# Optimization experiments

Hardware: AMD Instinct MI355X
Metric: run time of the kernel (lower is better)

Reference implementation:

```python
import jax, jax.numpy as jnp
import numpy as np

B, T, D, H, NB = 4, 2048, 128, 4, 2
DK = D // H
LN_EPS = 1e-3  # keras LayerNormalization default epsilon


def _pos_encoding(maxlen, d):
    # faithful to TransformerNet.get_position_encoding (flat pos-major layout)
    pe = np.array([pos / np.power(10000, 2 * i / d) for pos in range(maxlen) for i in range(d)])
    pe[::2] = np.sin(pe[::2])
    pe[1::2] = np.cos(pe[1::2])
    return jnp.asarray(pe.reshape(maxlen, d), dtype=jnp.float32)


def _ln(x, g, b):
    mu = jnp.mean(x, axis=-1, keepdims=True)
    var = jnp.mean(jnp.square(x - mu), axis=-1, keepdims=True)
    return g * (x - mu) / jnp.sqrt(var + LN_EPS) + b


def setup_inputs() -> dict:
    key = jax.random.key(0)
    ks = jax.random.split(key, 14)
    s = 1.0 / np.sqrt(D)
    w = lambda k, shape: (jax.random.normal(k, shape, jnp.float32) * s)
    return {
        'inputs': jax.random.normal(ks[0], (B, T, D), jnp.float32),
        'Wq': w(ks[1], (NB, D, D)), 'bq': jnp.zeros((NB, D), jnp.float32),
        'Wk': w(ks[2], (NB, D, D)), 'bk': jnp.zeros((NB, D), jnp.float32),
        'Wv': w(ks[3], (NB, D, D)), 'bv': jnp.zeros((NB, D), jnp.float32),
        'Wo': w(ks[4], (NB, D, D)), 'bo': jnp.zeros((NB, D), jnp.float32),
        'W1': w(ks[5], (NB, D, D)), 'b1': jnp.zeros((NB, D), jnp.float32),
        'W2': w(ks[6], (NB, D, D)), 'b2': jnp.zeros((NB, D), jnp.float32),
        'ln_g': jnp.ones((2 * NB, D), jnp.float32),
        'ln_b': jnp.zeros((2 * NB, D), jnp.float32),
    }


def reference(inputs, Wq, bq, Wk, bk, Wv, bv, Wo, bo, W1, b1, W2, b2, ln_g, ln_b):
    h = inputs + _pos_encoding(T, D)[None]  # [B,T,D]
    scale = 1.0 / jnp.sqrt(jnp.float32(DK))
    for i in range(NB):
        # pre-attention LayerNorm
        h = _ln(h, ln_g[2 * i], ln_b[2 * i])
        q = (h @ Wq[i] + bq[i]).reshape(B, T, H, DK)
        k = (h @ Wk[i] + bk[i]).reshape(B, T, H, DK)
        v = (h @ Wv[i] + bv[i]).reshape(B, T, H, DK)
        scores = jnp.einsum('bqhd,bkhd->bhqk', q, k) * scale
        p = jax.nn.softmax(scores, axis=-1)
        # mask is None in TransformerNet.call, but the renormalize step remains
        attn = p / (jnp.sum(p, axis=-1, keepdims=True) + 1e-8)
        ctx = jnp.einsum('bhqk,bkhd->bqhd', attn, v).reshape(B, T, D)
        h = ctx @ Wo[i] + bo[i]  # no residual around attention (as in source)
        # pre-FFN LayerNorm
        h = _ln(h, ln_g[2 * i + 1], ln_b[2 * i + 1])
        # FeedForward with internal residual
        h = h + (jnp.maximum(h @ W1[i] + b1[i], 0.0) @ W2[i] + b2[i])
    # final norm reuses norm_layers[-1] == norm_layers[2*NB-1] (source quirk)
    return _ln(h, ln_g[-1], ln_b[-1])
```

## Files before the change

kernel.cpp:

```cpp
#include <hip/hip_runtime.h>
#include <hip/hip_bf16.h>

typedef __bf16 bf16x8 __attribute__((ext_vector_type(8)));
typedef __bf16 bf16x4 __attribute__((ext_vector_type(4)));
typedef float f32x4 __attribute__((ext_vector_type(4)));
typedef float f32x16 __attribute__((ext_vector_type(16)));
typedef unsigned int u32x4v __attribute__((ext_vector_type(4)));

#define D_ 128
#define T_ 2048
#define B_ 4
#define H_ 4
#define NB_ 2


__global__ __launch_bounds__(256) void prep_weights(
    const float* __restrict__ Wq, const float* __restrict__ Wk,
    const float* __restrict__ Wv, const float* __restrict__ Wo,
    const float* __restrict__ W1, const float* __restrict__ W2,
    __bf16* __restrict__ wp)
{
  int tid = blockIdx.x * 256 + threadIdx.x;
  int e    = tid & 7;
  int lane = (tid >> 3) & 63;
  int ks   = (tid >> 9) & 3;
  int nt   = (tid >> 11) & 7;
  int i    = (tid >> 14) & (NB_ - 1);
  int j    = tid >> 15;
  int k = ks * 32 + (lane >> 4) * 8 + e;
  int n = nt * 16 + (lane & 15);
  const float* srcs[6] = {Wq, Wk, Wv, Wo, W1, W2};
  wp[tid] = (__bf16)srcs[j][i * 16384 + k * 128 + n];
}

__global__ __launch_bounds__(256) void posadd(
    const float* __restrict__ x, __bf16* __restrict__ hp)
{
  int w = threadIdx.x >> 6, lane = threadIdx.x & 63;
  int row = blockIdx.x * 4 + w;
  int t = row & (T_ - 1);
  #pragma unroll
  for (int e = 0; e < 2; e++) {
    int c = lane * 2 + e;
    float arg = (float)t * exp2f(-0.20762050593045952f * (float)c);
    float pe = (c & 1) ? cosf(arg) : sinf(arg);
    float v = x[row * D_ + c] + pe;
    size_t idx = ((size_t)(row >> 4) * 4 + (c >> 5)) * 512 +
                 ((row & 15) + 16 * ((c >> 3) & 3)) * 8 + (c & 7);
    hp[idx] = (__bf16)v;
  }
}

__global__ __launch_bounds__(256) void lnqkv(
    const __bf16* __restrict__ hp, const __bf16* __restrict__ wpq,
    const __bf16* __restrict__ wpk, const __bf16* __restrict__ wpv,
    const float* __restrict__ bq, const float* __restrict__ bk,
    const float* __restrict__ bv, const float* __restrict__ g,
    const float* __restrict__ beta,
    __bf16* __restrict__ qp, __bf16* __restrict__ kp, __bf16* __restrict__ vp)
{
  int w = threadIdx.x >> 6, lane = threadIdx.x & 63;
  int m0 = blockIdx.x * 16;
  int lr = lane & 15, kg = lane >> 4;

  bf16x8 araw[4];
  #pragma unroll
  for (int ks = 0; ks < 4; ks++)
    araw[ks] = *(const bf16x8*)(hp + ((size_t)blockIdx.x * 4 + ks) * 512 + lane * 8);

  float s = 0.f, s2 = 0.f;
  #pragma unroll
  for (int ks = 0; ks < 4; ks++)
    #pragma unroll
    for (int e = 0; e < 8; e++) {
      float x = (float)araw[ks][e];
      s += x; s2 += x * x;
    }
  s += __shfl_xor(s, 16, 64);  s2 += __shfl_xor(s2, 16, 64);
  s += __shfl_xor(s, 32, 64);  s2 += __shfl_xor(s2, 32, 64);
  float mu = s * (1.f / D_);
  float var = s2 * (1.f / D_) - mu * mu;
  float rstd = rsqrtf(var + 1e-3f);

  bf16x8 af[4];
  #pragma unroll
  for (int ks = 0; ks < 4; ks++) {
    int c0 = ks * 32 + kg * 8;
    float4 g0 = *(const float4*)(g + c0), g1 = *(const float4*)(g + c0 + 4);
    float4 q0 = *(const float4*)(beta + c0), q1 = *(const float4*)(beta + c0 + 4);
    const float* gp[2] = {&g0.x, &g1.x};
    const float* bp[2] = {&q0.x, &q1.x};
    #pragma unroll
    for (int e = 0; e < 8; e++)
      af[ks][e] = (__bf16)(((float)araw[ks][e] - mu) * rstd * gp[e >> 2][e & 3] + bp[e >> 2][e & 3]);
  }

  #pragma unroll
  for (int i = 0; i < 2; i++) {
    int nt = w * 2 + i;
    const __bf16* wq = wpq + (size_t)(nt * 4) * 512 + lane * 8;
    const __bf16* wk = wpk + (size_t)(nt * 4) * 512 + lane * 8;
    const __bf16* wv = wpv + (size_t)(nt * 4) * 512 + lane * 8;
    f32x4 aq = {0, 0, 0, 0}, ak = {0, 0, 0, 0}, av = {0, 0, 0, 0};
    #pragma unroll
    for (int ks = 0; ks < 4; ks++) {
      aq = __builtin_amdgcn_mfma_f32_16x16x32_bf16(af[ks], *(const bf16x8*)(wq + ks * 512), aq, 0, 0, 0);
      ak = __builtin_amdgcn_mfma_f32_16x16x32_bf16(af[ks], *(const bf16x8*)(wk + ks * 512), ak, 0, 0, 0);
      av = __builtin_amdgcn_mfma_f32_16x16x32_bf16(af[ks], *(const bf16x8*)(wv + ks * 512), av, 0, 0, 0);
    }
    int col = nt * 16 + lr;
    float bqc = bq[col], bkc = bk[col], bvc = bv[col];
    int dk = i * 16 + lr;
    int hi8 = (lr >> 3) & 1;
    #pragma unroll
    for (int r = 0; r < 4; r++) {
      int row = m0 + kg * 4 + r;
      int bb = row >> 11, tt = row & (T_ - 1);
      size_t qidx = ((((size_t)(bb * 64 + (tt >> 5)) * 4 + w) * 2 + i) * 512) +
                    ((tt & 31) + 32 * hi8) * 8 + (lr & 7);
      qp[qidx] = (__bf16)(aq[r] + bqc);
      size_t kidx = ((((size_t)(bb * 4 + w) * 64 + (tt >> 5)) * 2 + i) * 512) +
                    ((tt & 31) + 32 * hi8) * 8 + (lr & 7);
      kp[kidx] = (__bf16)(ak[r] + bkc);
      size_t vidx = ((((size_t)(bb * 4 + w) * 64 + (tt >> 5)) * 2 + ((tt >> 4) & 1)) * 512) +
                    (dk + 32 * ((tt >> 3) & 1)) * 8 + (tt & 7);
      vp[vidx] = (__bf16)(av[r] + bvc);
    }
  }
}

__global__ __launch_bounds__(256) void attn7(
    const __bf16* __restrict__ qp, const __bf16* __restrict__ kp,
    const __bf16* __restrict__ vp, __bf16* __restrict__ cp)
{
  __shared__ float mbuf[3][64][17];

  int w = threadIdx.x >> 6, lane = threadIdx.x & 63;
  int bh = blockIdx.x & 15, qt = blockIdx.x >> 4;
  int b = bh >> 2, h = bh & 3;
  int lq = lane & 31, hi = lane >> 5;

  const float qscale = 0.17677669529663687f * 1.4426950408889634f;
  const __bf16* qbase = qp + (((size_t)(b * 64 + qt) * 4 + h) * 2) * 512 + lane * 8;
  bf16x8 qraw0 = *(const bf16x8*)(qbase);
  bf16x8 qraw1 = *(const bf16x8*)(qbase + 512);
  bf16x8 qf0, qf1;
  #pragma unroll
  for (int e = 0; e < 8; e++) {
    qf0[e] = (__bf16)((float)qraw0[e] * qscale);
    qf1[e] = (__bf16)((float)qraw1[e] * qscale);
  }

  const __bf16* kbase = kp + ((size_t)(b * 4 + h) * 64) * 1024 + lane * 8;
  const __bf16* vbase = vp + ((size_t)(b * 4 + h) * 64) * 1024 + lane * 8;

  f32x16 acc;
  #pragma unroll
  for (int r = 0; r < 16; r++) acc[r] = 0.f;
  float l = 0.f;

  int kt = w * 16;
  bf16x8 kf0 = *(const bf16x8*)(kbase + (size_t)kt * 1024);
  bf16x8 kf1 = *(const bf16x8*)(kbase + (size_t)kt * 1024 + 512);
  bf16x8 vf0 = *(const bf16x8*)(vbase + (size_t)kt * 1024);
  bf16x8 vf1 = *(const bf16x8*)(vbase + (size_t)kt * 1024 + 512);

  for (int it = 0; it < 16; it++) {
    __builtin_amdgcn_s_setprio(1);
    f32x16 s;
    #pragma unroll
    for (int r = 0; r < 16; r++) s[r] = -24.f;
    s = __builtin_amdgcn_mfma_f32_32x32x16_bf16(kf0, qf0, s, 0, 0, 0);
    s = __builtin_amdgcn_mfma_f32_32x32x16_bf16(kf1, qf1, s, 0, 0, 0);
    __builtin_amdgcn_s_setprio(0);

    bf16x8 kn0, kn1, vn0, vn1;
    if (it < 15) {
      size_t nb = (size_t)(kt + 1) * 1024;
      kn0 = *(const bf16x8*)(kbase + nb);
      kn1 = *(const bf16x8*)(kbase + nb + 512);
      vn0 = *(const bf16x8*)(vbase + nb);
      vn1 = *(const bf16x8*)(vbase + nb + 512);
    }

    unsigned int aw[8];
    #pragma unroll
    for (int g = 0; g < 4; g++) {
      float p0 = __builtin_amdgcn_exp2f(s[g * 4 + 0]);
      float p1 = __builtin_amdgcn_exp2f(s[g * 4 + 1]);
      float p2 = __builtin_amdgcn_exp2f(s[g * 4 + 2]);
      float p3 = __builtin_amdgcn_exp2f(s[g * 4 + 3]);
      l += (p0 + p1) + (p2 + p3);
      unsigned int u01, u23;
      asm("v_cvt_pk_bf16_f32 %0, %1, %2" : "=v"(u01) : "v"(p0), "v"(p1));
      asm("v_cvt_pk_bf16_f32 %0, %1, %2" : "=v"(u23) : "v"(p2), "v"(p3));
      aw[g * 2] = u01; aw[g * 2 + 1] = u23;
    }
    unsigned int a0 = aw[0], a2 = aw[2];
    asm volatile("v_permlane32_swap_b32 %0, %1" : "+v"(a0), "+v"(a2));
    unsigned int a1 = aw[1], a3 = aw[3];
    asm volatile("v_permlane32_swap_b32 %0, %1" : "+v"(a1), "+v"(a3));
    bf16x8 pw0 = __builtin_bit_cast(bf16x8, (u32x4v){a0, a1, a2, a3});
    unsigned int a4 = aw[4], a6 = aw[6];
    asm volatile("v_permlane32_swap_b32 %0, %1" : "+v"(a4), "+v"(a6));
    unsigned int a5 = aw[5], a7 = aw[7];
    asm volatile("v_permlane32_swap_b32 %0, %1" : "+v"(a5), "+v"(a7));
    bf16x8 pw1 = __builtin_bit_cast(bf16x8, (u32x4v){a4, a5, a6, a7});

    __builtin_amdgcn_s_setprio(1);
    acc = __builtin_amdgcn_mfma_f32_32x32x16_bf16(vf0, pw0, acc, 0, 0, 0);
    acc = __builtin_amdgcn_mfma_f32_32x32x16_bf16(vf1, pw1, acc, 0, 0, 0);
    __builtin_amdgcn_s_setprio(0);

    kf0 = kn0; kf1 = kn1; vf0 = vn0; vf1 = vn1;
    kt += 1;
  }

  l += __shfl_xor(l, 32, 64);

  if (w > 0) {
    float* mb = &mbuf[w - 1][lane][0];
    #pragma unroll
    for (int r = 0; r < 16; r++) mb[r] = acc[r];
    mb[16] = l;
  }
  __syncthreads();
  if (w == 0) {
    #pragma unroll
    for (int w2_ = 0; w2_ < 3; w2_++) {
      const float* mb = &mbuf[w2_][lane][0];
      #pragma unroll
      for (int r = 0; r < 16; r++) acc[r] += mb[r];
      l += mb[16];
    }
    float inv = 1.f / l;
    __bf16* cbase = cp + ((size_t)(b * 128 + qt * 2 + (lq >> 4)) * 4 + h) * 512 + 4 * hi;
    #pragma unroll
    for (int g = 0; g < 4; g++) {
      bf16x4 o;
      #pragma unroll
      for (int j = 0; j < 4; j++) o[j] = (__bf16)(acc[g * 4 + j] * inv);
      *(bf16x4*)(cbase + ((lq & 15) + 16 * g) * 8) = o;
    }
  }
}

template <int LAST>
__global__ __launch_bounds__(256) void wo_ffn(
    const __bf16* __restrict__ cp, const __bf16* __restrict__ wpo,
    const float* __restrict__ bo, const float* __restrict__ g1,
    const float* __restrict__ bt1, const __bf16* __restrict__ wp1,
    const float* __restrict__ b1, const __bf16* __restrict__ wp2,
    const float* __restrict__ b2, const float* __restrict__ g2,
    const float* __restrict__ bt2, __bf16* __restrict__ hp,
    float* __restrict__ outf)
{
  __shared__ __attribute__((aligned(16))) __bf16 tb0[16][128];
  __shared__ __attribute__((aligned(16))) __bf16 tb1[16][128];
  __shared__ float2 statb[16][4];

  int w = threadIdx.x >> 6, lane = threadIdx.x & 63;
  int m0 = blockIdx.x * 16;
  int lr = lane & 15, kg = lane >> 4;
  int swz = (lr & 7) << 3;

  bf16x8 af[4];
  #pragma unroll
  for (int ks = 0; ks < 4; ks++)
    af[ks] = *(const bf16x8*)(cp + ((size_t)blockIdx.x * 4 + ks) * 512 + lane * 8);

  f32x4 acc[2] = {{0, 0, 0, 0}, {0, 0, 0, 0}};
  #pragma unroll
  for (int i = 0; i < 2; i++) {
    const __bf16* wrow = wpo + (size_t)((w * 2 + i) * 4) * 512 + lane * 8;
    #pragma unroll
    for (int ks = 0; ks < 4; ks++)
      acc[i] = __builtin_amdgcn_mfma_f32_16x16x32_bf16(af[ks], *(const bf16x8*)(wrow + ks * 512), acc[i], 0, 0, 0);
  }

  float xv[2][4];
  float s[4] = {0, 0, 0, 0}, s2[4] = {0, 0, 0, 0};
  #pragma unroll
  for (int i = 0; i < 2; i++) {
    float bcol = bo[(w * 2 + i) * 16 + lr];
    #pragma unroll
    for (int r = 0; r < 4; r++) {
      float y = acc[i][r] + bcol;
      xv[i][r] = y; s[r] += y; s2[r] += y * y;
    }
  }
  #pragma unroll
  for (int r = 0; r < 4; r++)
    for (int mk = 1; mk < 16; mk <<= 1) {
      s[r] += __shfl_xor(s[r], mk, 64);
      s2[r] += __shfl_xor(s2[r], mk, 64);
    }
  if (lr == 0) {
    #pragma unroll
    for (int r = 0; r < 4; r++) statb[kg * 4 + r][w] = make_float2(s[r], s2[r]);
  }
  __syncthreads();
  float mu_[4], rstd_[4];
  #pragma unroll
  for (int r = 0; r < 4; r++) {
    int row = kg * 4 + r;
    float ss = 0.f, ss2 = 0.f;
    #pragma unroll
    for (int w2 = 0; w2 < 4; w2++) {
      float2 t = statb[row][w2];
      ss += t.x; ss2 += t.y;
    }
    mu_[r] = ss * (1.f / D_);
    float var = ss2 * (1.f / D_) - mu_[r] * mu_[r];
    rstd_[r] = rsqrtf(var + 1e-3f);
  }
  float hres[2][4];
  #pragma unroll
  for (int i = 0; i < 2; i++) {
    int col = (w * 2 + i) * 16 + lr;
    float gc = g1[col], bc = bt1[col];
    #pragma unroll
    for (int r = 0; r < 4; r++) {
      float y = (xv[i][r] - mu_[r]) * rstd_[r] * gc + bc;
      hres[i][r] = y;
      int row = kg * 4 + r;
      tb0[row][col ^ ((row & 7) << 3)] = (__bf16)y;
    }
  }
  __syncthreads();

  bf16x8 a2[4];
  #pragma unroll
  for (int ks = 0; ks < 4; ks++)
    a2[ks] = *(const bf16x8*)(&tb0[lr][(ks * 32 + kg * 8) ^ swz]);
  f32x4 acc2[2] = {{0, 0, 0, 0}, {0, 0, 0, 0}};
  #pragma unroll
  for (int i = 0; i < 2; i++) {
    const __bf16* wrow = wp1 + (size_t)((w * 2 + i) * 4) * 512 + lane * 8;
    #pragma unroll
    for (int ks = 0; ks < 4; ks++)
      acc2[i] = __builtin_amdgcn_mfma_f32_16x16x32_bf16(a2[ks], *(const bf16x8*)(wrow + ks * 512), acc2[i], 0, 0, 0);
  }
  #pragma unroll
  for (int i = 0; i < 2; i++) {
    float bcol = b1[(w * 2 + i) * 16 + lr];
    int col = (w * 2 + i) * 16 + lr;
    #pragma unroll
    for (int r = 0; r < 4; r++) {
      int row = kg * 4 + r;
      tb1[row][col ^ ((row & 7) << 3)] = (__bf16)fmaxf(acc2[i][r] + bcol, 0.f);
    }
  }
  __syncthreads();

  bf16x8 a3[4];
  #pragma unroll
  for (int ks = 0; ks < 4; ks++)
    a3[ks] = *(const bf16x8*)(&tb1[lr][(ks * 32 + kg * 8) ^ swz]);
  f32x4 acc3[2] = {{0, 0, 0, 0}, {0, 0, 0, 0}};
  #pragma unroll
  for (int i = 0; i < 2; i++) {
    const __bf16* wrow = wp2 + (size_t)((w * 2 + i) * 4) * 512 + lane * 8;
    #pragma unroll
    for (int ks = 0; ks < 4; ks++)
      acc3[i] = __builtin_amdgcn_mfma_f32_16x16x32_bf16(a3[ks], *(const bf16x8*)(wrow + ks * 512), acc3[i], 0, 0, 0);
  }

  if constexpr (LAST) {
    float yv[2][4];
    float t[4] = {0, 0, 0, 0}, t2[4] = {0, 0, 0, 0};
    #pragma unroll
    for (int i = 0; i < 2; i++) {
      float bcol = b2[(w * 2 + i) * 16 + lr];
      #pragma unroll
      for (int r = 0; r < 4; r++) {
        float y = acc3[i][r] + bcol + hres[i][r];
        yv[i][r] = y; t[r] += y; t2[r] += y * y;
      }
    }
    #pragma unroll
    for (int r = 0; r < 4; r++)
      for (int mk = 1; mk < 16; mk <<= 1) {
        t[r] += __shfl_xor(t[r], mk, 64);
        t2[r] += __shfl_xor(t2[r], mk, 64);
      }
    __syncthreads();
    if (lr == 0) {
      #pragma unroll
      for (int r = 0; r < 4; r++) statb[kg * 4 + r][w] = make_float2(t[r], t2[r]);
    }
    __syncthreads();
    #pragma unroll
    for (int r = 0; r < 4; r++) {
      int row = kg * 4 + r;
      float ss = 0.f, ss2 = 0.f;
      #pragma unroll
      for (int w2 = 0; w2 < 4; w2++) {
        float2 tt = statb[row][w2];
        ss += tt.x; ss2 += tt.y;
      }
      float mu = ss * (1.f / D_);
      float var = ss2 * (1.f / D_) - mu * mu;
      float rstd = rsqrtf(var + 1e-3f);
      #pragma unroll
      for (int i = 0; i < 2; i++) {
        int col = (w * 2 + i) * 16 + lr;
        outf[(size_t)(m0 + row) * D_ + col] =
            (yv[i][r] - mu) * rstd * g2[col] + bt2[col];
      }
    }
  } else {
    #pragma unroll
    for (int i = 0; i < 2; i++) {
      int col = (w * 2 + i) * 16 + lr;
      float bcol = b2[col];
      size_t base = ((size_t)blockIdx.x * 4 + w) * 512 +
                    (size_t)16 * ((2 * i + (lr >> 3)) & 3) * 8 + (lr & 7);
      #pragma unroll
      for (int r = 0; r < 4; r++)
        hp[base + (kg * 4 + r) * 8] = (__bf16)(acc3[i][r] + bcol + hres[i][r]);
    }
  }
}

extern "C" void kernel_launch(void* const* d_in, const int* in_sizes, int n_in,
                              void* d_out, int out_size, void* d_ws, size_t ws_size,
                              hipStream_t stream)
{
  const float* inputs = (const float*)d_in[0];
  const float* Wq = (const float*)d_in[1];
  const float* bq = (const float*)d_in[2];
  const float* Wk = (const float*)d_in[3];
  const float* bk = (const float*)d_in[4];
  const float* Wv = (const float*)d_in[5];
  const float* bv = (const float*)d_in[6];
  const float* Wo = (const float*)d_in[7];
  const float* bo = (const float*)d_in[8];
  const float* W1 = (const float*)d_in[9];
  const float* b1 = (const float*)d_in[10];
  const float* W2 = (const float*)d_in[11];
  const float* b2 = (const float*)d_in[12];
  const float* ln_g = (const float*)d_in[13];
  const float* ln_b = (const float*)d_in[14];
  float* out = (float*)d_out;

  char* ws = (char*)d_ws;
  size_t off = 0;
  auto alloc = [&](size_t bytes) {
    void* p = ws + off;
    off = (off + bytes + 255) & ~(size_t)255;
    return p;
  };
  const size_t ACT = (size_t)8192 * 128 * sizeof(__bf16);
  __bf16* wp = (__bf16*)alloc((size_t)6 * NB_ * 16384 * sizeof(__bf16));
  __bf16* hp = (__bf16*)alloc(ACT);
  __bf16* qp = (__bf16*)alloc(ACT);
  __bf16* kp = (__bf16*)alloc(ACT);
  __bf16* vp = (__bf16*)alloc(ACT);
  __bf16* cb = (__bf16*)alloc(ACT);

  prep_weights<<<768, 256, 0, stream>>>(Wq, Wk, Wv, Wo, W1, W2, wp);
  posadd<<<2048, 256, 0, stream>>>(inputs, hp);

  for (int i = 0; i < NB_; i++) {
    const __bf16* wpq = wp + (size_t)(0 * NB_ + i) * 16384;
    const __bf16* wpk = wp + (size_t)(1 * NB_ + i) * 16384;
    const __bf16* wpv = wp + (size_t)(2 * NB_ + i) * 16384;
    const __bf16* wpo = wp + (size_t)(3 * NB_ + i) * 16384;
    const __bf16* wp1 = wp + (size_t)(4 * NB_ + i) * 16384;
    const __bf16* wp2 = wp + (size_t)(5 * NB_ + i) * 16384;

    lnqkv<<<512, 256, 0, stream>>>(hp, wpq, wpk, wpv,
                                   bq + i * 128, bk + i * 128, bv + i * 128,
                                   ln_g + (size_t)(2 * i) * 128, ln_b + (size_t)(2 * i) * 128,
                                   qp, kp, vp);
    attn7<<<1024, 256, 0, stream>>>(qp, kp, vp, cb);
    if (i == 0) {
      wo_ffn<0><<<512, 256, 0, stream>>>(cb, wpo, bo + i * 128,
                                         ln_g + 1 * 128, ln_b + 1 * 128,
                                         wp1, b1 + i * 128, wp2, b2 + i * 128,
                                         nullptr, nullptr, hp, nullptr);
    } else {
      wo_ffn<1><<<512, 256, 0, stream>>>(cb, wpo, bo + i * 128,
                                         ln_g + 3 * 128, ln_b + 3 * 128,
                                         wp1, b1 + i * 128, wp2, b2 + i * 128,
                                         ln_g + 3 * 128, ln_b + 3 * 128,
                                         nullptr, out);
    }
  }
}
```

Measured before the change: 157.1 us.

## Fuse block-0 FFN with block-1 LN+QKV and split attention keys over eight waves

The first block's Wo/FFN kernel now also runs the second block's pre-attention LayerNorm and Q/K/V projections. This drops one launch and the bf16 round trip of the hidden state through global memory. The attention kernel moves to 512 threads, splitting the key range over 8 waves of 8 tiles each instead of 4 waves of 16, to raise parallelism and shorten per-wave latency. The cost is a larger shared-memory reduction of eight partial accumulators, and a longer fused kernel that needs more registers.

```diff
diff --git a/kernel.cpp b/kernel.cpp
--- a/kernel.cpp
+++ b/kernel.cpp
@@ -129,11 +129,11 @@
   }
 }
 
-__global__ __launch_bounds__(256) void attn7(
+__global__ __launch_bounds__(512) void attn8(
     const __bf16* __restrict__ qp, const __bf16* __restrict__ kp,
     const __bf16* __restrict__ vp, __bf16* __restrict__ cp)
 {
-  __shared__ float mbuf[3][64][17];
+  __shared__ float mbuf[7][64][17];
 
   int w = threadIdx.x >> 6, lane = threadIdx.x & 63;
   int bh = blockIdx.x & 15, qt = blockIdx.x >> 4;
@@ -159,13 +159,13 @@
   for (int r = 0; r < 16; r++) acc[r] = 0.f;
   float l = 0.f;
 
-  int kt = w * 16;
+  int kt = w * 8;
   bf16x8 kf0 = *(const bf16x8*)(kbase + (size_t)kt * 1024);
   bf16x8 kf1 = *(const bf16x8*)(kbase + (size_t)kt * 1024 + 512);
   bf16x8 vf0 = *(const bf16x8*)(vbase + (size_t)kt * 1024);
   bf16x8 vf1 = *(const bf16x8*)(vbase + (size_t)kt * 1024 + 512);
 
-  for (int it = 0; it < 16; it++) {
+  for (int it = 0; it < 8; it++) {
     __builtin_amdgcn_s_setprio(1);
     f32x16 s;
     #pragma unroll
@@ -175,7 +175,7 @@
     __builtin_amdgcn_s_setprio(0);
 
     bf16x8 kn0, kn1, vn0, vn1;
-    if (it < 15) {
+    if (it < 7) {
       size_t nb = (size_t)(kt + 1) * 1024;
       kn0 = *(const bf16x8*)(kbase + nb);
       kn1 = *(const bf16x8*)(kbase + nb + 512);
@@ -227,7 +227,7 @@
   __syncthreads();
   if (w == 0) {
     #pragma unroll
-    for (int w2_ = 0; w2_ < 3; w2_++) {
+    for (int w2_ = 0; w2_ < 7; w2_++) {
       const float* mb = &mbuf[w2_][lane][0];
       #pragma unroll
       for (int r = 0; r < 16; r++) acc[r] += mb[r];
@@ -245,15 +245,214 @@
   }
 }
 
-template <int LAST>
-__global__ __launch_bounds__(256) void wo_ffn(
+__global__ __launch_bounds__(256) void wo_ffn_qkv(
+    const __bf16* __restrict__ cp, const __bf16* __restrict__ wpo,
+    const float* __restrict__ bo, const float* __restrict__ g1,
+    const float* __restrict__ bt1, const __bf16* __restrict__ wp1,
+    const float* __restrict__ b1, const __bf16* __restrict__ wp2,
+    const float* __restrict__ b2,
+    const float* __restrict__ gq, const float* __restrict__ btq,
+    const __bf16* __restrict__ wpq, const __bf16* __restrict__ wpk,
+    const __bf16* __restrict__ wpv,
+    const float* __restrict__ bq, const float* __restrict__ bk,
+    const float* __restrict__ bv,
+    __bf16* __restrict__ qp, __bf16* __restrict__ kp, __bf16* __restrict__ vp)
+{
+  __shared__ __attribute__((aligned(16))) __bf16 tb0[16][128];
+  __shared__ __attribute__((aligned(16))) __bf16 tb1[16][128];
+  __shared__ float2 statb[16][4];
+
+  int w = threadIdx.x >> 6, lane = threadIdx.x & 63;
+  int m0 = blockIdx.x * 16;
+  int lr = lane & 15, kg = lane >> 4;
+  int swz = (lr & 7) << 3;
+
+  bf16x8 af[4];
+  #pragma unroll
+  for (int ks = 0; ks < 4; ks++)
+    af[ks] = *(const bf16x8*)(cp + ((size_t)blockIdx.x * 4 + ks) * 512 + lane * 8);
+
+  f32x4 acc[2] = {{0, 0, 0, 0}, {0, 0, 0, 0}};
+  #pragma unroll
+  for (int i = 0; i < 2; i++) {
+    const __bf16* wrow = wpo + (size_t)((w * 2 + i) * 4) * 512 + lane * 8;
+    #pragma unroll
+    for (int ks = 0; ks < 4; ks++)
+      acc[i] = __builtin_amdgcn_mfma_f32_16x16x32_bf16(af[ks], *(const bf16x8*)(wrow + ks * 512), acc[i], 0, 0, 0);
+  }
+
+  float xv[2][4];
+  float s[4] = {0, 0, 0, 0}, s2[4] = {0, 0, 0, 0};
+  #pragma unroll
+  for (int i = 0; i < 2; i++) {
+    float bcol = bo[(w * 2 + i) * 16 + lr];
+    #pragma unroll
+    for (int r = 0; r < 4; r++) {
+      float y = acc[i][r] + bcol;
+      xv[i][r] = y; s[r] += y; s2[r] += y * y;
+    }
+  }
+  #pragma unroll
+  for (int r = 0; r < 4; r++)
+    for (int mk = 1; mk < 16; mk <<= 1) {
+      s[r] += __shfl_xor(s[r], mk, 64);
+      s2[r] += __shfl_xor(s2[r], mk, 64);
+    }
+  if (lr == 0) {
+    #pragma unroll
+    for (int r = 0; r < 4; r++) statb[kg * 4 + r][w] = make_float2(s[r], s2[r]);
+  }
+  __syncthreads();
+  float mu_[4], rstd_[4];
+  #pragma unroll
+  for (int r = 0; r < 4; r++) {
+    int row = kg * 4 + r;
+    float ss = 0.f, ss2 = 0.f;
+    #pragma unroll
+    for (int w2 = 0; w2 < 4; w2++) {
+      float2 t = statb[row][w2];
+      ss += t.x; ss2 += t.y;
+    }
+    mu_[r] = ss * (1.f / D_);
+    float var = ss2 * (1.f / D_) - mu_[r] * mu_[r];
+    rstd_[r] = rsqrtf(var + 1e-3f);
+  }
+  float hres[2][4];
+  #pragma unroll
+  for (int i = 0; i < 2; i++) {
+    int col = (w * 2 + i) * 16 + lr;
+    float gc = g1[col], bc = bt1[col];
+    #pragma unroll
+    for (int r = 0; r < 4; r++) {
+      float y = (xv[i][r] - mu_[r]) * rstd_[r] * gc + bc;
+      hres[i][r] = y;
+      int row = kg * 4 + r;
+      tb0[row][col ^ ((row & 7) << 3)] = (__bf16)y;
+    }
+  }
+  __syncthreads();
+
+  bf16x8 a2[4];
+  #pragma unroll
+  for (int ks = 0; ks < 4; ks++)
+    a2[ks] = *(const bf16x8*)(&tb0[lr][(ks * 32 + kg * 8) ^ swz]);
+  f32x4 acc2[2] = {{0, 0, 0, 0}, {0, 0, 0, 0}};
+  #pragma unroll
+  for (int i = 0; i < 2; i++) {
+    const __bf16* wrow = wp1 + (size_t)((w * 2 + i) * 4) * 512 + lane * 8;
+    #pragma unroll
+    for (int ks = 0; ks < 4; ks++)
+      acc2[i] = __builtin_amdgcn_mfma_f32_16x16x32_bf16(a2[ks], *(const bf16x8*)(wrow + ks * 512), acc2[i], 0, 0, 0);
+  }
+  #pragma unroll
+  for (int i = 0; i < 2; i++) {
+    float bcol = b1[(w * 2 + i) * 16 + lr];
+    int col = (w * 2 + i) * 16 + lr;
+    #pragma unroll
+    for (int r = 0; r < 4; r++) {
+      int row = kg * 4 + r;
+      tb1[row][col ^ ((row & 7) << 3)] = (__bf16)fmaxf(acc2[i][r] + bcol, 0.f);
+    }
+  }
+  __syncthreads();
+
+  bf16x8 a3[4];
+  #pragma unroll
+  for (int ks = 0; ks < 4; ks++)
+    a3[ks] = *(const bf16x8*)(&tb1[lr][(ks * 32 + kg * 8) ^ swz]);
+  f32x4 acc3[2] = {{0, 0, 0, 0}, {0, 0, 0, 0}};
+  #pragma unroll
+  for (int i = 0; i < 2; i++) {
+    const __bf16* wrow = wp2 + (size_t)((w * 2 + i) * 4) * 512 + lane * 8;
+    #pragma unroll
+    for (int ks = 0; ks < 4; ks++)
+      acc3[i] = __builtin_amdgcn_mfma_f32_16x16x32_bf16(a3[ks], *(const bf16x8*)(wrow + ks * 512), acc3[i], 0, 0, 0);
+  }
+
+  #pragma unroll
+  for (int i = 0; i < 2; i++) {
+    int col = (w * 2 + i) * 16 + lr;
+    float bcol = b2[col];
+    #pragma unroll
+    for (int r = 0; r < 4; r++) {
+      int row = kg * 4 + r;
+      tb0[row][col ^ ((row & 7) << 3)] = (__bf16)(acc3[i][r] + bcol + hres[i][r]);
+    }
+  }
+  __syncthreads();
+
+  bf16x8 araw[4];
+  #pragma unroll
+  for (int ks = 0; ks < 4; ks++)
+    araw[ks] = *(const bf16x8*)(&tb0[lr][(ks * 32 + kg * 8) ^ swz]);
+  float t = 0.f, t2 = 0.f;
+  #pragma unroll
+  for (int ks = 0; ks < 4; ks++)
+    #pragma unroll
+    for (int e = 0; e < 8; e++) {
+      float x = (float)araw[ks][e];
+      t += x; t2 += x * x;
+    }
+  t += __shfl_xor(t, 16, 64);  t2 += __shfl_xor(t2, 16, 64);
+  t += __shfl_xor(t, 32, 64);  t2 += __shfl_xor(t2, 32, 64);
+  float mu = t * (1.f / D_);
+  float var = t2 * (1.f / D_) - mu * mu;
+  float rstd = rsqrtf(var + 1e-3f);
+
+  bf16x8 af2[4];
+  #pragma unroll
+  for (int ks = 0; ks < 4; ks++) {
+    int c0 = ks * 32 + kg * 8;
+    float4 g0 = *(const float4*)(gq + c0), g1v = *(const float4*)(gq + c0 + 4);
+    float4 q0 = *(const float4*)(btq + c0), q1 = *(const float4*)(btq + c0 + 4);
+    const float* gp[2] = {&g0.x, &g1v.x};
+    const float* bp[2] = {&q0.x, &q1.x};
+    #pragma unroll
+    for (int e = 0; e < 8; e++)
+      af2[ks][e] = (__bf16)(((float)araw[ks][e] - mu) * rstd * gp[e >> 2][e & 3] + bp[e >> 2][e & 3]);
+  }
+
+  #pragma unroll
+  for (int i = 0; i < 2; i++) {
+    int nt = w * 2 + i;
+    const __bf16* wq = wpq + (size_t)(nt * 4) * 512 + lane * 8;
+    const __bf16* wk = wpk + (size_t)(nt * 4) * 512 + lane * 8;
+    const __bf16* wv = wpv + (size_t)(nt * 4) * 512 + lane * 8;
+    f32x4 aq = {0, 0, 0, 0}, ak = {0, 0, 0, 0}, av = {0, 0, 0, 0};
+    #pragma unroll
+    for (int ks = 0; ks < 4; ks++) {
+      aq = __builtin_amdgcn_mfma_f32_16x16x32_bf16(af2[ks], *(const bf16x8*)(wq + ks * 512), aq, 0, 0, 0);
+      ak = __builtin_amdgcn_mfma_f32_16x16x32_bf16(af2[ks], *(const bf16x8*)(wk + ks * 512), ak, 0, 0, 0);
+      av = __builtin_amdgcn_mfma_f32_16x16x32_bf16(af2[ks], *(const bf16x8*)(wv + ks * 512), av, 0, 0, 0);
+    }
+    int col = nt * 16 + lr;
+    float bqc = bq[col], bkc = bk[col], bvc = bv[col];
+    int dk = i * 16 + lr;
+    int hi8 = (lr >> 3) & 1;
+    #pragma unroll
+    for (int r = 0; r < 4; r++) {
+      int row = m0 + kg * 4 + r;
+      int bb = row >> 11, tt = row & (T_ - 1);
+      size_t qidx = ((((size_t)(bb * 64 + (tt >> 5)) * 4 + w) * 2 + i) * 512) +
+                    ((tt & 31) + 32 * hi8) * 8 + (lr & 7);
+      qp[qidx] = (__bf16)(aq[r] + bqc);
+      size_t kidx = ((((size_t)(bb * 4 + w) * 64 + (tt >> 5)) * 2 + i) * 512) +
+                    ((tt & 31) + 32 * hi8) * 8 + (lr & 7);
+      kp[kidx] = (__bf16)(ak[r] + bkc);
+      size_t vidx = ((((size_t)(bb * 4 + w) * 64 + (tt >> 5)) * 2 + ((tt >> 4) & 1)) * 512) +
+                    (dk + 32 * ((tt >> 3) & 1)) * 8 + (tt & 7);
+      vp[vidx] = (__bf16)(av[r] + bvc);
+    }
+  }
+}
+
+__global__ __launch_bounds__(256) void wo_ffn_last(
     const __bf16* __restrict__ cp, const __bf16* __restrict__ wpo,
     const float* __restrict__ bo, const float* __restrict__ g1,
     const float* __restrict__ bt1, const __bf16* __restrict__ wp1,
     const float* __restrict__ b1, const __bf16* __restrict__ wp2,
     const float* __restrict__ b2, const float* __restrict__ g2,
-    const float* __restrict__ bt2, __bf16* __restrict__ hp,
-    float* __restrict__ outf)
+    const float* __restrict__ bt2, float* __restrict__ outf)
 {
   __shared__ __attribute__((aligned(16))) __bf16 tb0[16][128];
   __shared__ __attribute__((aligned(16))) __bf16 tb1[16][128];
@@ -366,59 +565,46 @@
       acc3[i] = __builtin_amdgcn_mfma_f32_16x16x32_bf16(a3[ks], *(const bf16x8*)(wrow + ks * 512), acc3[i], 0, 0, 0);
   }
 
-  if constexpr (LAST) {
-    float yv[2][4];
-    float t[4] = {0, 0, 0, 0}, t2[4] = {0, 0, 0, 0};
-    #pragma unroll
-    for (int i = 0; i < 2; i++) {
-      float bcol = b2[(w * 2 + i) * 16 + lr];
-      #pragma unroll
-      for (int r = 0; r < 4; r++) {
-        float y = acc3[i][r] + bcol + hres[i][r];
-        yv[i][r] = y; t[r] += y; t2[r] += y * y;
-      }
-    }
-    #pragma unroll
-    for (int r = 0; r < 4; r++)
-      for (int mk = 1; mk < 16; mk <<= 1) {
-        t[r] += __shfl_xor(t[r], mk, 64);
-        t2[r] += __shfl_xor(t2[r], mk, 64);
-      }
-    __syncthreads();
-    if (lr == 0) {
-      #pragma unroll
-      for (int r = 0; r < 4; r++) statb[kg * 4 + r][w] = make_float2(t[r], t2[r]);
-    }
-    __syncthreads();
-    #pragma unroll
-    for (int r = 0; r < 4; r++) {
-      int row = kg * 4 + r;
-      float ss = 0.f, ss2 = 0.f;
-      #pragma unroll
-      for (int w2 = 0; w2 < 4; w2++) {
-        float2 tt = statb[row][w2];
-        ss += tt.x; ss2 += tt.y;
-      }
-      float mu = ss * (1.f / D_);
-      float var = ss2 * (1.f / D_) - mu * mu;
-      float rstd = rsqrtf(var + 1e-3f);
-      #pragma unroll
-      for (int i = 0; i < 2; i++) {
-        int col = (w * 2 + i) * 16 + lr;
-        outf[(size_t)(m0 + row) * D_ + col] =
-            (yv[i][r] - mu) * rstd * g2[col] + bt2[col];
-      }
-    }
-  } else {
+  float yv[2][4];
+  float t[4] = {0, 0, 0, 0}, t2[4] = {0, 0, 0, 0};
+  #pragma unroll
+  for (int i = 0; i < 2; i++) {
+    float bcol = b2[(w * 2 + i) * 16 + lr];
+    #pragma unroll
+    for (int r = 0; r < 4; r++) {
+      float y = acc3[i][r] + bcol + hres[i][r];
+      yv[i][r] = y; t[r] += y; t2[r] += y * y;
+    }
+  }
+  #pragma unroll
+  for (int r = 0; r < 4; r++)
+    for (int mk = 1; mk < 16; mk <<= 1) {
+      t[r] += __shfl_xor(t[r], mk, 64);
+      t2[r] += __shfl_xor(t2[r], mk, 64);
+    }
+  __syncthreads();
+  if (lr == 0) {
+    #pragma unroll
+    for (int r = 0; r < 4; r++) statb[kg * 4 + r][w] = make_float2(t[r], t2[r]);
+  }
+  __syncthreads();
+  #pragma unroll
+  for (int r = 0; r < 4; r++) {
+    int row = kg * 4 + r;
+    float ss = 0.f, ss2 = 0.f;
+    #pragma unroll
+    for (int w2 = 0; w2 < 4; w2++) {
+      float2 tt = statb[row][w2];
+      ss += tt.x; ss2 += tt.y;
+    }
+    float mu = ss * (1.f / D_);
+    float var = ss2 * (1.f / D_) - mu * mu;
+    float rstd = rsqrtf(var + 1e-3f);
     #pragma unroll
     for (int i = 0; i < 2; i++) {
       int col = (w * 2 + i) * 16 + lr;
-      float bcol = b2[col];
-      size_t base = ((size_t)blockIdx.x * 4 + w) * 512 +
-                    (size_t)16 * ((2 * i + (lr >> 3)) & 3) * 8 + (lr & 7);
-      #pragma unroll
-      for (int r = 0; r < 4; r++)
-        hp[base + (kg * 4 + r) * 8] = (__bf16)(acc3[i][r] + bcol + hres[i][r]);
+      outf[(size_t)(m0 + row) * D_ + col] =
+          (yv[i][r] - mu) * rstd * g2[col] + bt2[col];
     }
   }
 }
@@ -462,30 +648,31 @@
   prep_weights<<<768, 256, 0, stream>>>(Wq, Wk, Wv, Wo, W1, W2, wp);
   posadd<<<2048, 256, 0, stream>>>(inputs, hp);
 
-  for (int i = 0; i < NB_; i++) {
-    const __bf16* wpq = wp + (size_t)(0 * NB_ + i) * 16384;
-    const __bf16* wpk = wp + (size_t)(1 * NB_ + i) * 16384;
-    const __bf16* wpv = wp + (size_t)(2 * NB_ + i) * 16384;
-    const __bf16* wpo = wp + (size_t)(3 * NB_ + i) * 16384;
-    const __bf16* wp1 = wp + (size_t)(4 * NB_ + i) * 16384;
-    const __bf16* wp2 = wp + (size_t)(5 * NB_ + i) * 16384;
-
-    lnqkv<<<512, 256, 0, stream>>>(hp, wpq, wpk, wpv,
-                                   bq + i * 128, bk + i * 128, bv + i * 128,
-                                   ln_g + (size_t)(2 * i) * 128, ln_b + (size_t)(2 * i) * 128,
-                                   qp, kp, vp);
-    attn7<<<1024, 256, 0, stream>>>(qp, kp, vp, cb);
-    if (i == 0) {
-      wo_ffn<0><<<512, 256, 0, stream>>>(cb, wpo, bo + i * 128,
-                                         ln_g + 1 * 128, ln_b + 1 * 128,
-                                         wp1, b1 + i * 128, wp2, b2 + i * 128,
-                                         nullptr, nullptr, hp, nullptr);
-    } else {
-      wo_ffn<1><<<512, 256, 0, stream>>>(cb, wpo, bo + i * 128,
-                                         ln_g + 3 * 128, ln_b + 3 * 128,
-                                         wp1, b1 + i * 128, wp2, b2 + i * 128,
-                                         ln_g + 3 * 128, ln_b + 3 * 128,
-                                         nullptr, out);
-    }
-  }
+  const __bf16* wpq0 = wp + (size_t)(0 * NB_ + 0) * 16384;
+  const __bf16* wpk0 = wp + (size_t)(1 * NB_ + 0) * 16384;
+  const __bf16* wpv0 = wp + (size_t)(2 * NB_ + 0) * 16384;
+  const __bf16* wpo0 = wp + (size_t)(3 * NB_ + 0) * 16384;
+  const __bf16* wp10 = wp + (size_t)(4 * NB_ + 0) * 16384;
+  const __bf16* wp20 = wp + (size_t)(5 * NB_ + 0) * 16384;
+  const __bf16* wpq1 = wp + (size_t)(0 * NB_ + 1) * 16384;
+  const __bf16* wpk1 = wp + (size_t)(1 * NB_ + 1) * 16384;
+  const __bf16* wpv1 = wp + (size_t)(2 * NB_ + 1) * 16384;
+  const __bf16* wpo1 = wp + (size_t)(3 * NB_ + 1) * 16384;
+  const __bf16* wp11 = wp + (size_t)(4 * NB_ + 1) * 16384;
+  const __bf16* wp21 = wp + (size_t)(5 * NB_ + 1) * 16384;
+
+  lnqkv<<<512, 256, 0, stream>>>(hp, wpq0, wpk0, wpv0, bq, bk, bv,
+                                 ln_g, ln_b, qp, kp, vp);
+  attn8<<<1024, 512, 0, stream>>>(qp, kp, vp, cb);
+  wo_ffn_qkv<<<512, 256, 0, stream>>>(cb, wpo0, bo,
+                                      ln_g + 128, ln_b + 128, wp10, b1, wp20, b2,
+                                      ln_g + 2 * 128, ln_b + 2 * 128,
+                                      wpq1, wpk1, wpv1,
+                                      bq + 128, bk + 128, bv + 128,
+                                      qp, kp, vp);
+  attn8<<<1024, 512, 0, stream>>>(qp, kp, vp, cb);
+  wo_ffn_last<<<512, 256, 0, stream>>>(cb, wpo1, bo + 128,
+                                       ln_g + 3 * 128, ln_b + 3 * 128,
+                                       wp11, b1 + 128, wp21, b2 + 128,
+                                       ln_g + 3 * 128, ln_b + 3 * 128, out);
 }
```

After: 148.3 us. 1.06x faster.
